# Optimization experiments

Hardware: AMD Instinct MI355X
Metric: run time of the kernel (lower is better)

Reference implementation:

```python
import math
import jax, jax.numpy as jnp
import numpy as np

NUM_BUCKETS = 32
MAX_DISTANCE = 128
N_HEADS = 16
D_KV = 64


def _relative_position_bucket(relative_position, num_buckets=NUM_BUCKETS, max_distance=MAX_DISTANCE):
    # bidirectional variant (encoder): half the buckets for each sign
    nb = num_buckets // 2
    n = -relative_position
    ret = (n < 0).astype(jnp.int32) * nb
    n = jnp.abs(n)
    max_exact = nb // 2
    is_small = n < max_exact
    val_if_large = max_exact + (
        jnp.log(jnp.maximum(n, 1).astype(jnp.float32) / max_exact)
        / math.log(max_distance / max_exact)
        * (nb - max_exact)
    ).astype(jnp.int32)
    val_if_large = jnp.minimum(val_if_large, nb - 1)
    return ret + jnp.where(is_small, n, val_if_large)


def setup_inputs() -> dict:
    key = jax.random.key(0)
    ks = jax.random.split(key, 6)
    d_model = 1024
    inner = N_HEADS * D_KV
    scale = 1.0 / math.sqrt(d_model)
    x = jax.random.normal(ks[0], (2, 2048, d_model), dtype=jnp.float32)
    wq = jax.random.normal(ks[1], (d_model, inner), dtype=jnp.float32) * scale
    wk = jax.random.normal(ks[2], (d_model, inner), dtype=jnp.float32) * scale
    wv = jax.random.normal(ks[3], (d_model, inner), dtype=jnp.float32) * scale
    wo = jax.random.normal(ks[4], (inner, d_model), dtype=jnp.float32) * scale
    rel_emb = jax.random.normal(ks[5], (NUM_BUCKETS, N_HEADS), dtype=jnp.float32)
    return {"x": x, "wq": wq, "wk": wk, "wv": wv, "wo": wo, "rel_emb": rel_emb}


def reference(x, wq, wk, wv, wo, rel_emb):
    B, S, D = x.shape
    # QKV projections (no bias, T5 style), split heads -> [B, S, H, Dk]
    q = (x @ wq).reshape(B, S, N_HEADS, D_KV)
    k = (x @ wk).reshape(B, S, N_HEADS, D_KV)
    v = (x @ wv).reshape(B, S, N_HEADS, D_KV)
    # NOTE: T5 does NOT scale by 1/sqrt(d_kv)
    scores = jnp.einsum("bqhd,bkhd->bhqk", q, k)  # [B, H, S, S]
    # relative position bias
    ctx = jnp.arange(S)[:, None]
    mem = jnp.arange(S)[None, :]
    buckets = _relative_position_bucket(mem - ctx)  # [S, S]
    bias = rel_emb[buckets]  # [S, S, H]
    bias = jnp.transpose(bias, (2, 0, 1))[None]  # [1, H, S, S]
    scores = scores + bias
    weights = jax.nn.softmax(scores.astype(jnp.float32), axis=-1).astype(scores.dtype)
    context = jnp.einsum("bhqk,bkhd->bqhd", weights, v).reshape(B, S, N_HEADS * D_KV)
    return context @ wo
```

## Files before the change

### kernel.cpp

```cpp
#include <hip/hip_runtime.h>
#include <hip/hip_bf16.h>

typedef __attribute__((ext_vector_type(8))) _Float16 f16x8;
typedef __attribute__((ext_vector_type(4))) float f32x4;
typedef unsigned short u16;
typedef unsigned int u32;

#define S_LEN 2048
#define NH    16
#define DK    64
#define DMODEL 1024
#define LSTR  40

union F16U { _Float16 h; u16 u; };
__device__ __forceinline__ u16 f2h(float f) {
    F16U v; v.h = (_Float16)f; return v.u;
}

__global__ __launch_bounds__(256) void bias_table_kernel(
    const float* __restrict__ rel_emb, float* __restrict__ tab)
{
    int idx = blockIdx.x * 256 + threadIdx.x;
    int h = idx >> 12;
    int t = idx & 4095;
    int rp = t - 2048;
    int n = -rp;
    int ret = 0;
    if (n < 0) { ret = 16; n = -n; }
    int inner;
    if (n < 8) {
        inner = n;
    } else {
        inner = 8 + (n >= 12) + (n >= 16) + (n >= 23) + (n >= 32)
                  + (n >= 46) + (n >= 64) + (n >= 91);
        if (inner > 15) inner = 15;
    }
    tab[h * 4096 + t] = rel_emb[(ret + inner) * NH + h];
}

__global__ __launch_bounds__(256) void convert_x(
    const float* __restrict__ X, u16* __restrict__ Xf)
{
    long i8 = ((long)blockIdx.x * 256 + threadIdx.x) * 8;
    float4 a = *(const float4*)&X[i8];
    float4 b = *(const float4*)&X[i8 + 4];
    *(ushort4*)&Xf[i8] =
        make_ushort4(f2h(a.x), f2h(a.y), f2h(a.z), f2h(a.w));
    *(ushort4*)&Xf[i8 + 4] =
        make_ushort4(f2h(b.x), f2h(b.y), f2h(b.z), f2h(b.w));
}

__global__ __launch_bounds__(256) void convert_wT(
    const float* __restrict__ Wq, const float* __restrict__ Wk,
    const float* __restrict__ Wv, const float* __restrict__ Wo,
    u16* __restrict__ WT)
{
    const float* src = (blockIdx.z == 0) ? Wq : (blockIdx.z == 1) ? Wk
                     : (blockIdx.z == 2) ? Wv : Wo;
    u16* dT = WT + (long)blockIdx.z * 1048576;
    __shared__ __align__(16) float T[64 * 68];
    const int k0 = blockIdx.y * 64, n0 = blockIdx.x * 64;
    const int tid = threadIdx.x;
    #pragma unroll
    for (int u = 0; u < 4; u++) {
        int w = tid + u * 256;
        int r = w >> 4, c4 = (w & 15) * 4;
        *(float4*)&T[r * 68 + c4] =
            *(const float4*)&src[(long)(k0 + r) * DMODEL + n0 + c4];
    }
    __syncthreads();
    #pragma unroll
    for (int u = 0; u < 4; u++) {
        int w = tid + u * 256;
        int n = w >> 4, kc = (w & 15) * 4;
        *(ushort4*)&dT[(long)(n0 + n) * DMODEL + k0 + kc] = make_ushort4(
            f2h(T[(kc + 0) * 68 + n]), f2h(T[(kc + 1) * 68 + n]),
            f2h(T[(kc + 2) * 68 + n]), f2h(T[(kc + 3) * 68 + n]));
    }
}

__global__ __launch_bounds__(256, 3) void gemm_qkv_mfma(
    const u16* __restrict__ Xf, const u16* __restrict__ WT,
    u16* __restrict__ Qf, u16* __restrict__ Kf, u16* __restrict__ VT)
{
    const int z = blockIdx.z;
    const u16* BT = WT + (long)z * 1048576;

    __shared__ __align__(16) u16 Ah[128 * LSTR], Bh[128 * LSTR];

    const int tid = threadIdx.x;
    const int wv = tid >> 6, lane = tid & 63;
    const int g = lane >> 4, li = lane & 15;
    const int wr = wv >> 1, wc = wv & 1;
    const int bm = blockIdx.y * 128, bn = blockIdx.x * 128;

    f32x4 acc[4][4];
    #pragma unroll
    for (int i = 0; i < 4; i++)
        #pragma unroll
        for (int j = 0; j < 4; j++) acc[i][j] = (f32x4){0.f, 0.f, 0.f, 0.f};

    for (int k0 = 0; k0 < DMODEL; k0 += 32) {
        #pragma unroll
        for (int u = 0; u < 2; u++) {
            int w = tid + u * 256;
            int row = w >> 2, q8 = (w & 3) * 8;
            *(uint4*)&Ah[row * LSTR + q8] =
                *(const uint4*)&Xf[(long)(bm + row) * DMODEL + k0 + q8];
            *(uint4*)&Bh[row * LSTR + q8] =
                *(const uint4*)&BT[(long)(bn + row) * DMODEL + k0 + q8];
        }
        __syncthreads();

        f16x8 a_h[4], b_h[4];
        #pragma unroll
        for (int i = 0; i < 4; i++)
            a_h[i] = *(const f16x8*)&Ah[(wr * 64 + i * 16 + li) * LSTR + g * 8];
        #pragma unroll
        for (int j = 0; j < 4; j++)
            b_h[j] = *(const f16x8*)&Bh[(wc * 64 + j * 16 + li) * LSTR + g * 8];
        #pragma unroll
        for (int i = 0; i < 4; i++)
            #pragma unroll
            for (int j = 0; j < 4; j++)
                acc[i][j] = __builtin_amdgcn_mfma_f32_16x16x32_f16(
                    a_h[i], b_h[j], acc[i][j], 0, 0, 0);
        __syncthreads();
    }

    if (z == 2) {
        #pragma unroll
        for (int i = 0; i < 4; i++) {
            int s_base = bm + wr * 64 + i * 16 + g * 4;
            int bb = s_base >> 11, s = s_base & 2047;
            #pragma unroll
            for (int j = 0; j < 4; j++) {
                int gcol = bn + wc * 64 + j * 16 + li;
                int hh = gcol >> 6, d = gcol & 63;
                long idx = (((long)(bb * NH + hh)) * DK + d) * S_LEN + s;
                *(ushort4*)&VT[idx] = make_ushort4(
                    f2h(acc[i][j][0]), f2h(acc[i][j][1]),
                    f2h(acc[i][j][2]), f2h(acc[i][j][3]));
            }
        }
    } else {
        u16* O = (z == 0) ? Qf : Kf;
        #pragma unroll
        for (int i = 0; i < 4; i++) {
            #pragma unroll
            for (int r = 0; r < 4; r++) {
                int grow = bm + wr * 64 + i * 16 + g * 4 + r;
                int bb = grow >> 11, s = grow & 2047;
                #pragma unroll
                for (int j = 0; j < 4; j++) {
                    int gcol = bn + wc * 64 + j * 16 + li;
                    int hh = gcol >> 6, d = gcol & 63;
                    long idx = (((long)(bb * NH + hh)) * S_LEN + s) * DK + d;
                    O[idx] = f2h(acc[i][j][r]);
                }
            }
        }
    }
}

__global__ __launch_bounds__(256, 3) void gemm_out_mfma(
    const u16* __restrict__ Ab, const u16* __restrict__ WT,
    float* __restrict__ O)
{
    const u16* BT = WT + 3L * 1048576;
    __shared__ __align__(16) u16 Ah[128 * LSTR], Bh[128 * LSTR];

    const int tid = threadIdx.x;
    const int wv = tid >> 6, lane = tid & 63;
    const int g = lane >> 4, li = lane & 15;
    const int wr = wv >> 1, wc = wv & 1;
    const int bm = blockIdx.y * 128, bn = blockIdx.x * 128;

    f32x4 acc[4][4];
    #pragma unroll
    for (int i = 0; i < 4; i++)
        #pragma unroll
        for (int j = 0; j < 4; j++) acc[i][j] = (f32x4){0.f, 0.f, 0.f, 0.f};

    for (int k0 = 0; k0 < DMODEL; k0 += 32) {
        #pragma unroll
        for (int u = 0; u < 2; u++) {
            int w = tid + u * 256;
            int row = w >> 2, q8 = (w & 3) * 8;
            *(uint4*)&Ah[row * LSTR + q8] =
                *(const uint4*)&Ab[(long)(bm + row) * DMODEL + k0 + q8];
            *(uint4*)&Bh[row * LSTR + q8] =
                *(const uint4*)&BT[(long)(bn + row) * DMODEL + k0 + q8];
        }
        __syncthreads();

        f16x8 a_h[4], b_h[4];
        #pragma unroll
        for (int i = 0; i < 4; i++)
            a_h[i] = *(const f16x8*)&Ah[(wr * 64 + i * 16 + li) * LSTR + g * 8];
        #pragma unroll
        for (int j = 0; j < 4; j++)
            b_h[j] = *(const f16x8*)&Bh[(wc * 64 + j * 16 + li) * LSTR + g * 8];
        #pragma unroll
        for (int i = 0; i < 4; i++)
            #pragma unroll
            for (int j = 0; j < 4; j++)
                acc[i][j] = __builtin_amdgcn_mfma_f32_16x16x32_f16(
                    a_h[i], b_h[j], acc[i][j], 0, 0, 0);
        __syncthreads();
    }

    #pragma unroll
    for (int i = 0; i < 4; i++)
        #pragma unroll
        for (int r = 0; r < 4; r++) {
            int grow = bm + wr * 64 + i * 16 + g * 4 + r;
            #pragma unroll
            for (int j = 0; j < 4; j++) {
                int gcol = bn + wc * 64 + j * 16 + li;
                O[(long)grow * DMODEL + gcol] = acc[i][j][r];
            }
        }
}

#define APAD 72

__global__ __launch_bounds__(256, 5) void attn_mfma(
    const u16* __restrict__ Qf, const u16* __restrict__ Kf,
    const u16* __restrict__ VT, const float* __restrict__ tab,
    u16* __restrict__ ctxb)
{
    __shared__ __align__(16) u16 Ks[64 * APAD];
    __shared__ __align__(16) u16 Vs[64 * APAD];
    __shared__ __align__(16) u16 Ps[64 * APAD];
    __shared__ float biasS[128];

    const int tid = threadIdx.x;
    const int wv = tid >> 6, lane = tid & 63;
    const int g = lane >> 4, li = lane & 15;
    const int qblk = blockIdx.x & 31;
    const int h = (blockIdx.x >> 5) & 15;
    const int b = blockIdx.x >> 9;
    const int q0 = qblk * 64;
    const long bh = b * NH + h;
    const int qloc = wv * 16 + li;

    const u16* KhG = Kf + bh * (S_LEN * DK);
    const u16* VtG = VT + bh * (DK * S_LEN);
    const float* th = tab + h * 4096;

    f16x8 q0f, q1f;
    {
        long qrow = bh * S_LEN + q0 + qloc;
        const u16* ph = Qf + qrow * DK + g * 8;
        q0f = *(const f16x8*)ph;  q1f = *(const f16x8*)(ph + 32);
    }

    f32x4 Oc[4];
    #pragma unroll
    for (int n = 0; n < 4; n++) Oc[n] = (f32x4){0.f, 0.f, 0.f, 0.f};
    float mP = -1e30f, lR = 0.f;

    for (int kt0 = 0; kt0 < S_LEN; kt0 += 64) {
        #pragma unroll
        for (int u = 0; u < 2; u++) {
            int w = tid + u * 256;
            int row = w >> 3, c8 = (w & 7) * 8;
            *(uint4*)&Ks[row * APAD + c8] =
                *(const uint4*)&KhG[(long)(kt0 + row) * DK + c8];
            *(uint4*)&Vs[row * APAD + c8] =
                *(const uint4*)&VtG[(long)row * S_LEN + kt0 + c8];
        }
        if (tid < 128) {
            int idx = kt0 + tid - 63 - q0 + 2048;
            idx = idx < 0 ? 0 : (idx > 4095 ? 4095 : idx);
            biasS[tid] = th[idx];
        }
        __syncthreads();

        f32x4 Sa[4];
        #pragma unroll
        for (int m = 0; m < 4; m++) {
            const u16* kp = &Ks[(m * 16 + li) * APAD + g * 8];
            f16x8 k0 = *(const f16x8*)kp, k1 = *(const f16x8*)(kp + 32);
            f32x4 s = (f32x4){0.f, 0.f, 0.f, 0.f};
            s = __builtin_amdgcn_mfma_f32_16x16x32_f16(k0, q0f, s, 0, 0, 0);
            s = __builtin_amdgcn_mfma_f32_16x16x32_f16(k1, q1f, s, 0, 0, 0);
            Sa[m] = s;
        }

        #pragma unroll
        for (int m = 0; m < 4; m++)
            #pragma unroll
            for (int r = 0; r < 4; r++)
                Sa[m][r] += biasS[m * 16 + g * 4 + r + 63 - qloc];

        float pm = Sa[0][0];
        #pragma unroll
        for (int m = 0; m < 4; m++)
            #pragma unroll
            for (int r = 0; r < 4; r++) pm = fmaxf(pm, Sa[m][r]);
        pm = fmaxf(pm, __shfl_xor(pm, 16));
        pm = fmaxf(pm, __shfl_xor(pm, 32));

        float mn = fmaxf(mP, pm);
        float alpha = __expf(mP - mn);
        mP = mn;

        float ls = 0.f;
        #pragma unroll
        for (int m = 0; m < 4; m++)
            #pragma unroll
            for (int r = 0; r < 4; r++) {
                Sa[m][r] = __expf(Sa[m][r] - mn);
                ls += Sa[m][r];
            }
        ls += __shfl_xor(ls, 16);
        ls += __shfl_xor(ls, 32);
        lR = lR * alpha + ls;

        float aO[4];
        #pragma unroll
        for (int r = 0; r < 4; r++) aO[r] = __shfl(alpha, g * 4 + r);
        #pragma unroll
        for (int n = 0; n < 4; n++)
            #pragma unroll
            for (int r = 0; r < 4; r++) Oc[n][r] *= aO[r];

        #pragma unroll
        for (int m = 0; m < 4; m++)
            *(ushort4*)&Ps[qloc * APAD + m * 16 + g * 4] = make_ushort4(
                f2h(Sa[m][0]), f2h(Sa[m][1]), f2h(Sa[m][2]), f2h(Sa[m][3]));

        {
            const u16* pp = &Ps[qloc * APAD + g * 8];
            f16x8 p0 = *(const f16x8*)pp, p1 = *(const f16x8*)(pp + 32);
            #pragma unroll
            for (int n = 0; n < 4; n++) {
                const u16* vp = &Vs[(n * 16 + li) * APAD + g * 8];
                f16x8 v0 = *(const f16x8*)vp, v1 = *(const f16x8*)(vp + 32);
                Oc[n] = __builtin_amdgcn_mfma_f32_16x16x32_f16(p0, v0, Oc[n], 0, 0, 0);
                Oc[n] = __builtin_amdgcn_mfma_f32_16x16x32_f16(p1, v1, Oc[n], 0, 0, 0);
            }
        }
        __syncthreads();
    }

    float linv = 1.0f / lR;
    float iv[4];
    #pragma unroll
    for (int r = 0; r < 4; r++) iv[r] = __shfl(linv, g * 4 + r);
    #pragma unroll
    for (int n = 0; n < 4; n++)
        #pragma unroll
        for (int r = 0; r < 4; r++)
            ctxb[((long)(b * S_LEN + q0 + wv * 16 + g * 4 + r)) * DMODEL
                 + h * DK + n * 16 + li] = f2h(Oc[n][r] * iv[r]);
}

extern "C" void kernel_launch(void* const* d_in, const int* in_sizes, int n_in,
                              void* d_out, int out_size, void* d_ws, size_t ws_size,
                              hipStream_t stream)
{
    const float* x    = (const float*)d_in[0];
    const float* wq   = (const float*)d_in[1];
    const float* wk   = (const float*)d_in[2];
    const float* wv   = (const float*)d_in[3];
    const float* wo   = (const float*)d_in[4];
    const float* rel  = (const float*)d_in[5];

    u16* W0 = (u16*)d_ws;
    u16* Xf  = W0;
    u16* Qf  = W0 + 4194304;
    u16* Kf  = W0 + 8388608;
    u16* VT  = W0 + 12582912;
    u16* WT  = W0 + 16777216;
    float* tab = (float*)(W0 + 20971520);
    u16* ctxb = Xf;

    bias_table_kernel<<<dim3(256), dim3(256), 0, stream>>>(rel, tab);
    convert_x<<<dim3(2048), dim3(256), 0, stream>>>(x, Xf);
    convert_wT<<<dim3(16, 16, 4), dim3(256), 0, stream>>>(wq, wk, wv, wo, WT);
    gemm_qkv_mfma<<<dim3(8, 32, 3), dim3(256), 0, stream>>>(Xf, WT, Qf, Kf, VT);
    attn_mfma<<<dim3(1024), dim3(256), 0, stream>>>(Qf, Kf, VT, tab, ctxb);
    gemm_out_mfma<<<dim3(8, 32), dim3(256), 0, stream>>>(ctxb, WT, (float*)d_out);
}
```

Baseline: 241.0 us.

## Fuse prep kernels, vectorize GEMM epilogues, and prefetch K/V in attention

Merges the bias-table, x-conversion and weight-transpose kernels into a single prep launch. The GEMMs swap their MFMA operands so each lane holds four contiguous columns, which lets the Q/K and output epilogues use vector stores instead of scalar ones. The attention kernel preloads the whole bias slice it needs into LDS once, register-prefetches the next K/V tile while computing the current one, uses packed round-toward-zero fp16 conversion for P, and applies the rescale with an fma onto a fresh accumulator. Occupancy is lowered to 4 blocks because LDS use is larger, and register pressure rises from the prefetch registers.

```diff
diff --git a/kernel.cpp b/kernel.cpp
--- a/kernel.cpp
+++ b/kernel.cpp
@@ -2,6 +2,7 @@
 #include <hip/hip_bf16.h>
 
 typedef __attribute__((ext_vector_type(8))) _Float16 f16x8;
+typedef __attribute__((ext_vector_type(2))) __fp16 fp16x2;
 typedef __attribute__((ext_vector_type(4))) float f32x4;
 typedef unsigned short u16;
 typedef unsigned int u32;
@@ -16,66 +17,68 @@
 __device__ __forceinline__ u16 f2h(float f) {
     F16U v; v.h = (_Float16)f; return v.u;
 }
-
-__global__ __launch_bounds__(256) void bias_table_kernel(
-    const float* __restrict__ rel_emb, float* __restrict__ tab)
-{
-    int idx = blockIdx.x * 256 + threadIdx.x;
-    int h = idx >> 12;
-    int t = idx & 4095;
-    int rp = t - 2048;
-    int n = -rp;
-    int ret = 0;
-    if (n < 0) { ret = 16; n = -n; }
-    int inner;
-    if (n < 8) {
-        inner = n;
-    } else {
-        inner = 8 + (n >= 12) + (n >= 16) + (n >= 23) + (n >= 32)
-                  + (n >= 46) + (n >= 64) + (n >= 91);
-        if (inner > 15) inner = 15;
-    }
-    tab[h * 4096 + t] = rel_emb[(ret + inner) * NH + h];
-}
-
-__global__ __launch_bounds__(256) void convert_x(
-    const float* __restrict__ X, u16* __restrict__ Xf)
-{
-    long i8 = ((long)blockIdx.x * 256 + threadIdx.x) * 8;
-    float4 a = *(const float4*)&X[i8];
-    float4 b = *(const float4*)&X[i8 + 4];
-    *(ushort4*)&Xf[i8] =
-        make_ushort4(f2h(a.x), f2h(a.y), f2h(a.z), f2h(a.w));
-    *(ushort4*)&Xf[i8 + 4] =
-        make_ushort4(f2h(b.x), f2h(b.y), f2h(b.z), f2h(b.w));
-}
-
-__global__ __launch_bounds__(256) void convert_wT(
+union PKU { fp16x2 h; u32 u; };
+__device__ __forceinline__ u32 pkrtz(float a, float b) {
+    PKU v; v.h = __builtin_amdgcn_cvt_pkrtz(a, b); return v.u;
+}
+
+__global__ __launch_bounds__(256) void prep_kernel(
+    const float* __restrict__ x,
     const float* __restrict__ Wq, const float* __restrict__ Wk,
     const float* __restrict__ Wv, const float* __restrict__ Wo,
-    u16* __restrict__ WT)
+    const float* __restrict__ rel_emb,
+    u16* __restrict__ Xf, u16* __restrict__ WT, float* __restrict__ tab)
 {
-    const float* src = (blockIdx.z == 0) ? Wq : (blockIdx.z == 1) ? Wk
-                     : (blockIdx.z == 2) ? Wv : Wo;
-    u16* dT = WT + (long)blockIdx.z * 1048576;
     __shared__ __align__(16) float T[64 * 68];
-    const int k0 = blockIdx.y * 64, n0 = blockIdx.x * 64;
+    const int blk = blockIdx.x;
     const int tid = threadIdx.x;
-    #pragma unroll
-    for (int u = 0; u < 4; u++) {
-        int w = tid + u * 256;
-        int r = w >> 4, c4 = (w & 15) * 4;
-        *(float4*)&T[r * 68 + c4] =
-            *(const float4*)&src[(long)(k0 + r) * DMODEL + n0 + c4];
-    }
-    __syncthreads();
-    #pragma unroll
-    for (int u = 0; u < 4; u++) {
-        int w = tid + u * 256;
-        int n = w >> 4, kc = (w & 15) * 4;
-        *(ushort4*)&dT[(long)(n0 + n) * DMODEL + k0 + kc] = make_ushort4(
-            f2h(T[(kc + 0) * 68 + n]), f2h(T[(kc + 1) * 68 + n]),
-            f2h(T[(kc + 2) * 68 + n]), f2h(T[(kc + 3) * 68 + n]));
+
+    if (blk < 2048) {
+        long i8 = ((long)blk * 256 + tid) * 8;
+        float4 a = *(const float4*)&x[i8];
+        float4 b = *(const float4*)&x[i8 + 4];
+        *(ushort4*)&Xf[i8] =
+            make_ushort4(f2h(a.x), f2h(a.y), f2h(a.z), f2h(a.w));
+        *(ushort4*)&Xf[i8 + 4] =
+            make_ushort4(f2h(b.x), f2h(b.y), f2h(b.z), f2h(b.w));
+    } else if (blk < 3072) {
+        int id = blk - 2048;
+        int z = id >> 8, rem = id & 255;
+        int k0 = (rem >> 4) * 64, n0 = (rem & 15) * 64;
+        const float* src = (z == 0) ? Wq : (z == 1) ? Wk : (z == 2) ? Wv : Wo;
+        u16* dT = WT + (long)z * 1048576;
+        #pragma unroll
+        for (int u = 0; u < 4; u++) {
+            int w = tid + u * 256;
+            int r = w >> 4, c4 = (w & 15) * 4;
+            *(float4*)&T[r * 68 + c4] =
+                *(const float4*)&src[(long)(k0 + r) * DMODEL + n0 + c4];
+        }
+        __syncthreads();
+        #pragma unroll
+        for (int u = 0; u < 4; u++) {
+            int w = tid + u * 256;
+            int n = w >> 4, kc = (w & 15) * 4;
+            *(ushort4*)&dT[(long)(n0 + n) * DMODEL + k0 + kc] = make_ushort4(
+                f2h(T[(kc + 0) * 68 + n]), f2h(T[(kc + 1) * 68 + n]),
+                f2h(T[(kc + 2) * 68 + n]), f2h(T[(kc + 3) * 68 + n]));
+        }
+    } else {
+        int idx = (blk - 3072) * 256 + tid;
+        int h = idx >> 12;
+        int t = idx & 4095;
+        int n = -(t - 2048);
+        int ret = 0;
+        if (n < 0) { ret = 16; n = -n; }
+        int inner;
+        if (n < 8) {
+            inner = n;
+        } else {
+            inner = 8 + (n >= 12) + (n >= 16) + (n >= 23) + (n >= 32)
+                      + (n >= 46) + (n >= 64) + (n >= 91);
+            if (inner > 15) inner = 15;
+        }
+        tab[h * 4096 + t] = rel_emb[(ret + inner) * NH + h];
     }
 }
 
@@ -119,12 +122,21 @@
         #pragma unroll
         for (int j = 0; j < 4; j++)
             b_h[j] = *(const f16x8*)&Bh[(wc * 64 + j * 16 + li) * LSTR + g * 8];
-        #pragma unroll
-        for (int i = 0; i < 4; i++)
-            #pragma unroll
-            for (int j = 0; j < 4; j++)
-                acc[i][j] = __builtin_amdgcn_mfma_f32_16x16x32_f16(
-                    a_h[i], b_h[j], acc[i][j], 0, 0, 0);
+        if (z == 2) {
+            #pragma unroll
+            for (int i = 0; i < 4; i++)
+                #pragma unroll
+                for (int j = 0; j < 4; j++)
+                    acc[i][j] = __builtin_amdgcn_mfma_f32_16x16x32_f16(
+                        a_h[i], b_h[j], acc[i][j], 0, 0, 0);
+        } else {
+            #pragma unroll
+            for (int i = 0; i < 4; i++)
+                #pragma unroll
+                for (int j = 0; j < 4; j++)
+                    acc[i][j] = __builtin_amdgcn_mfma_f32_16x16x32_f16(
+                        b_h[j], a_h[i], acc[i][j], 0, 0, 0);
+        }
         __syncthreads();
     }
 
@@ -147,17 +159,16 @@
         u16* O = (z == 0) ? Qf : Kf;
         #pragma unroll
         for (int i = 0; i < 4; i++) {
-            #pragma unroll
-            for (int r = 0; r < 4; r++) {
-                int grow = bm + wr * 64 + i * 16 + g * 4 + r;
-                int bb = grow >> 11, s = grow & 2047;
-                #pragma unroll
-                for (int j = 0; j < 4; j++) {
-                    int gcol = bn + wc * 64 + j * 16 + li;
-                    int hh = gcol >> 6, d = gcol & 63;
-                    long idx = (((long)(bb * NH + hh)) * S_LEN + s) * DK + d;
-                    O[idx] = f2h(acc[i][j][r]);
-                }
+            int srow = bm + wr * 64 + i * 16 + li;
+            int bb = srow >> 11, s = srow & 2047;
+            #pragma unroll
+            for (int j = 0; j < 4; j++) {
+                int dcol = bn + wc * 64 + j * 16 + g * 4;
+                int hh = dcol >> 6, d = dcol & 63;
+                long idx = (((long)(bb * NH + hh)) * S_LEN + s) * DK + d;
+                *(ushort4*)&O[idx] = make_ushort4(
+                    f2h(acc[i][j][0]), f2h(acc[i][j][1]),
+                    f2h(acc[i][j][2]), f2h(acc[i][j][3]));
             }
         }
     }
@@ -206,26 +217,26 @@
             #pragma unroll
             for (int j = 0; j < 4; j++)
                 acc[i][j] = __builtin_amdgcn_mfma_f32_16x16x32_f16(
-                    a_h[i], b_h[j], acc[i][j], 0, 0, 0);
-        __syncthreads();
-    }
-
-    #pragma unroll
-    for (int i = 0; i < 4; i++)
-        #pragma unroll
-        for (int r = 0; r < 4; r++) {
-            int grow = bm + wr * 64 + i * 16 + g * 4 + r;
-            #pragma unroll
-            for (int j = 0; j < 4; j++) {
-                int gcol = bn + wc * 64 + j * 16 + li;
-                O[(long)grow * DMODEL + gcol] = acc[i][j][r];
-            }
-        }
+                    b_h[j], a_h[i], acc[i][j], 0, 0, 0);
+        __syncthreads();
+    }
+
+    #pragma unroll
+    for (int i = 0; i < 4; i++) {
+        int grow = bm + wr * 64 + i * 16 + li;
+        #pragma unroll
+        for (int j = 0; j < 4; j++) {
+            int gcol = bn + wc * 64 + j * 16 + g * 4;
+            *(float4*)&O[(long)grow * DMODEL + gcol] = make_float4(
+                acc[i][j][0], acc[i][j][1], acc[i][j][2], acc[i][j][3]);
+        }
+    }
 }
 
 #define APAD 72
-
-__global__ __launch_bounds__(256, 5) void attn_mfma(
+#define BIAS_LEN 2112
+
+__global__ __launch_bounds__(256, 4) void attn_mfma(
     const u16* __restrict__ Qf, const u16* __restrict__ Kf,
     const u16* __restrict__ VT, const float* __restrict__ tab,
     u16* __restrict__ ctxb)
@@ -233,7 +244,7 @@
     __shared__ __align__(16) u16 Ks[64 * APAD];
     __shared__ __align__(16) u16 Vs[64 * APAD];
     __shared__ __align__(16) u16 Ps[64 * APAD];
-    __shared__ float biasS[128];
+    __shared__ float biasL[BIAS_LEN];
 
     const int tid = threadIdx.x;
     const int wv = tid >> 6, lane = tid & 63;
@@ -249,6 +260,11 @@
     const u16* VtG = VT + bh * (DK * S_LEN);
     const float* th = tab + h * 4096;
 
+    {
+        const float* tb = th + 2048 - q0 - 63;
+        for (int j = tid; j < BIAS_LEN; j += 256) biasL[j] = tb[j];
+    }
+
     f16x8 q0f, q1f;
     {
         long qrow = bh * S_LEN + q0 + qloc;
@@ -261,22 +277,28 @@
     for (int n = 0; n < 4; n++) Oc[n] = (f32x4){0.f, 0.f, 0.f, 0.f};
     float mP = -1e30f, lR = 0.f;
 
+    const int srow = tid >> 3, sc8 = (tid & 7) * 8;
+    const int srow1 = srow + 32;
+    uint4 kreg0, kreg1, vreg0, vreg1;
+    kreg0 = *(const uint4*)&KhG[(long)srow * DK + sc8];
+    kreg1 = *(const uint4*)&KhG[(long)srow1 * DK + sc8];
+    vreg0 = *(const uint4*)&VtG[(long)srow * S_LEN + sc8];
+    vreg1 = *(const uint4*)&VtG[(long)srow1 * S_LEN + sc8];
+
     for (int kt0 = 0; kt0 < S_LEN; kt0 += 64) {
-        #pragma unroll
-        for (int u = 0; u < 2; u++) {
-            int w = tid + u * 256;
-            int row = w >> 3, c8 = (w & 7) * 8;
-            *(uint4*)&Ks[row * APAD + c8] =
-                *(const uint4*)&KhG[(long)(kt0 + row) * DK + c8];
-            *(uint4*)&Vs[row * APAD + c8] =
-                *(const uint4*)&VtG[(long)row * S_LEN + kt0 + c8];
-        }
-        if (tid < 128) {
-            int idx = kt0 + tid - 63 - q0 + 2048;
-            idx = idx < 0 ? 0 : (idx > 4095 ? 4095 : idx);
-            biasS[tid] = th[idx];
-        }
-        __syncthreads();
+        *(uint4*)&Ks[srow * APAD + sc8]  = kreg0;
+        *(uint4*)&Ks[srow1 * APAD + sc8] = kreg1;
+        *(uint4*)&Vs[srow * APAD + sc8]  = vreg0;
+        *(uint4*)&Vs[srow1 * APAD + sc8] = vreg1;
+        __syncthreads();
+
+        int nt = kt0 + 64;
+        if (nt < S_LEN) {
+            kreg0 = *(const uint4*)&KhG[(long)(nt + srow) * DK + sc8];
+            kreg1 = *(const uint4*)&KhG[(long)(nt + srow1) * DK + sc8];
+            vreg0 = *(const uint4*)&VtG[(long)srow * S_LEN + nt + sc8];
+            vreg1 = *(const uint4*)&VtG[(long)srow1 * S_LEN + nt + sc8];
+        }
 
         f32x4 Sa[4];
         #pragma unroll
@@ -289,11 +311,12 @@
             Sa[m] = s;
         }
 
+        const int jb = kt0 + g * 4 + 63 - qloc;
         #pragma unroll
         for (int m = 0; m < 4; m++)
             #pragma unroll
             for (int r = 0; r < 4; r++)
-                Sa[m][r] += biasS[m * 16 + g * 4 + r + 63 - qloc];
+                Sa[m][r] += biasL[jb + m * 16 + r];
 
         float pm = Sa[0][0];
         #pragma unroll
@@ -306,6 +329,9 @@
         float mn = fmaxf(mP, pm);
         float alpha = __expf(mP - mn);
         mP = mn;
+        float aO[4];
+        #pragma unroll
+        for (int r = 0; r < 4; r++) aO[r] = __shfl(alpha, g * 4 + r);
 
         float ls = 0.f;
         #pragma unroll
@@ -319,19 +345,16 @@
         ls += __shfl_xor(ls, 32);
         lR = lR * alpha + ls;
 
-        float aO[4];
-        #pragma unroll
-        for (int r = 0; r < 4; r++) aO[r] = __shfl(alpha, g * 4 + r);
-        #pragma unroll
-        for (int n = 0; n < 4; n++)
-            #pragma unroll
-            for (int r = 0; r < 4; r++) Oc[n][r] *= aO[r];
-
-        #pragma unroll
-        for (int m = 0; m < 4; m++)
-            *(ushort4*)&Ps[qloc * APAD + m * 16 + g * 4] = make_ushort4(
-                f2h(Sa[m][0]), f2h(Sa[m][1]), f2h(Sa[m][2]), f2h(Sa[m][3]));
-
+        #pragma unroll
+        for (int m = 0; m < 4; m++) {
+            u32 lo = pkrtz(Sa[m][0], Sa[m][1]);
+            u32 hi = pkrtz(Sa[m][2], Sa[m][3]);
+            *(uint2*)&Ps[qloc * APAD + m * 16 + g * 4] = make_uint2(lo, hi);
+        }
+
+        f32x4 Tc[4];
+        #pragma unroll
+        for (int n = 0; n < 4; n++) Tc[n] = (f32x4){0.f, 0.f, 0.f, 0.f};
         {
             const u16* pp = &Ps[qloc * APAD + g * 8];
             f16x8 p0 = *(const f16x8*)pp, p1 = *(const f16x8*)(pp + 32);
@@ -339,10 +362,16 @@
             for (int n = 0; n < 4; n++) {
                 const u16* vp = &Vs[(n * 16 + li) * APAD + g * 8];
                 f16x8 v0 = *(const f16x8*)vp, v1 = *(const f16x8*)(vp + 32);
-                Oc[n] = __builtin_amdgcn_mfma_f32_16x16x32_f16(p0, v0, Oc[n], 0, 0, 0);
-                Oc[n] = __builtin_amdgcn_mfma_f32_16x16x32_f16(p1, v1, Oc[n], 0, 0, 0);
+                Tc[n] = __builtin_amdgcn_mfma_f32_16x16x32_f16(p0, v0, Tc[n], 0, 0, 0);
+                Tc[n] = __builtin_amdgcn_mfma_f32_16x16x32_f16(p1, v1, Tc[n], 0, 0, 0);
             }
         }
+        #pragma unroll
+        for (int n = 0; n < 4; n++)
+            #pragma unroll
+            for (int r = 0; r < 4; r++)
+                Oc[n][r] = fmaf(Oc[n][r], aO[r], Tc[n][r]);
+
         __syncthreads();
     }
 
@@ -378,9 +407,8 @@
     float* tab = (float*)(W0 + 20971520);
     u16* ctxb = Xf;
 
-    bias_table_kernel<<<dim3(256), dim3(256), 0, stream>>>(rel, tab);
-    convert_x<<<dim3(2048), dim3(256), 0, stream>>>(x, Xf);
-    convert_wT<<<dim3(16, 16, 4), dim3(256), 0, stream>>>(wq, wk, wv, wo, WT);
+    prep_kernel<<<dim3(3328), dim3(256), 0, stream>>>(x, wq, wk, wv, wo, rel,
+                                                      Xf, WT, tab);
     gemm_qkv_mfma<<<dim3(8, 32, 3), dim3(256), 0, stream>>>(Xf, WT, Qf, Kf, VT);
     attn_mfma<<<dim3(1024), dim3(256), 0, stream>>>(Qf, Kf, VT, tab, ctxb);
     gemm_out_mfma<<<dim3(8, 32), dim3(256), 0, stream>>>(ctxb, WT, (float*)d_out);
```

Result: slower. 296.7 us (+23.1%).
